# Performance work log

Hardware: AMD Instinct MI355X
Metric: run time of the kernel (lower is better)

The kernel has to match this reference:

```python
import jax, jax.numpy as jnp
import numpy as np
from jax import lax

B, H, W, CIN = 16, 96, 320, 32
N_ACTIVE = 200000
COUT = 256
FC_IN = (H // 8) * (W // 8) * 128  # 12*40*128 = 61440


def _conv(x, w, b):
    # stride-2, pad-1, 3x3 conv in NCHW / OIHW layout
    y = lax.conv_general_dilated(x, w, (2, 2), [(1, 1), (1, 1)],
                                 dimension_numbers=('NCHW', 'OIHW', 'NCHW'))
    return y + b[None, :, None, None]


def _maxpool3(x):
    # 3x3 maxpool, stride 1, pad 1 (NCHW)
    return lax.reduce_window(x, -jnp.inf, lax.max,
                             (1, 1, 3, 3), (1, 1, 1, 1),
                             [(0, 0), (0, 0), (1, 1), (1, 1)])


def setup_inputs() -> dict:
    key = jax.random.key(0)
    ks = jax.random.split(key, 12)
    input_feat = jax.random.normal(ks[0], (B, H, W, CIN), dtype=jnp.float32)
    cb = jax.random.randint(ks[1], (N_ACTIVE, 1), 0, B)
    cy = jax.random.randint(ks[2], (N_ACTIVE, 1), 0, H)
    cx = jax.random.randint(ks[3], (N_ACTIVE, 1), 0, W)
    spconv_coords = jnp.concatenate([cb, cy, cx], axis=1).astype(jnp.int32)
    w1 = jax.random.normal(ks[4], (32, CIN, 3, 3), dtype=jnp.float32) * (1.0 / np.sqrt(CIN * 9))
    b1 = jax.random.normal(ks[5], (32,), dtype=jnp.float32) * 0.01
    w2 = jax.random.normal(ks[6], (64, 32, 3, 3), dtype=jnp.float32) * (1.0 / np.sqrt(32 * 9))
    b2 = jax.random.normal(ks[7], (64,), dtype=jnp.float32) * 0.01
    w3 = jax.random.normal(ks[8], (128, 64, 3, 3), dtype=jnp.float32) * (1.0 / np.sqrt(64 * 9))
    b3 = jax.random.normal(ks[9], (128,), dtype=jnp.float32) * 0.01
    fc_w = jax.random.normal(ks[10], (COUT, FC_IN), dtype=jnp.float32) * (1.0 / np.sqrt(FC_IN))
    fc_b = jax.random.normal(ks[11], (COUT,), dtype=jnp.float32) * 0.01
    return {"input_feat": input_feat, "spconv_coords": spconv_coords,
            "w1": w1, "b1": b1, "w2": w2, "b2": b2, "w3": w3, "b3": b3,
            "fc_w": fc_w, "fc_b": fc_b}


def reference(input_feat, spconv_coords, w1, b1, w2, b2, w3, b3, fc_w, fc_b):
    bi = spconv_coords[:, 0]
    yi = spconv_coords[:, 1]
    xi = spconv_coords[:, 2]
    # gather active-site features, then scatter into a dense NHWC grid
    feats = input_feat[bi, yi, xi]                       # [N, CIN]
    dense = jnp.zeros_like(input_feat).at[bi, yi, xi].set(feats)
    x = dense.transpose(0, 3, 1, 2)                      # [B, CIN, H, W]
    x = jax.nn.relu(_maxpool3(_conv(x, w1, b1)))         # [B, 32, H/2, W/2]
    x = jax.nn.relu(_maxpool3(_conv(x, w2, b2)))         # [B, 64, H/4, W/4]
    x = jax.nn.relu(_maxpool3(_conv(x, w3, b3)))         # [B, 128, H/8, W/8]
    x = x.reshape(x.shape[0], -1)                        # [B, FC_IN]
    return jax.nn.relu(x @ fc_w.T + fc_b)                # [B, COUT]
```

## Files before the change

kernel.cpp:

```cpp
#include <hip/hip_runtime.h>

#define NB 16
#define NH 96
#define NW 320
#define NCIN 32

#define FC_K 61440
#define FC_KB 128
#define FC_NKC 480

typedef __attribute__((ext_vector_type(8))) short short8;
typedef __attribute__((ext_vector_type(4))) float f32x4;

__device__ inline unsigned short f2bf(float f) {
    union { float f; unsigned int u; } v; v.f = f;
    unsigned int r = v.u + 0x7FFF + ((v.u >> 16) & 1);
    return (unsigned short)(r >> 16);
}
__device__ inline float bf2f(unsigned short s) {
    union { unsigned int u; float f; } v; v.u = ((unsigned int)s) << 16; return v.f;
}
__device__ inline unsigned short fhi(float f) {
    union { float f; unsigned int u; } v; v.f = f; return (unsigned short)(v.u >> 16);
}

__global__ __launch_bounds__(256) void setup_all(const float* __restrict__ w1,
                                                 const float* __restrict__ w2,
                                                 const float* __restrict__ w3,
                                                 unsigned short* __restrict__ f1,
                                                 unsigned short* __restrict__ f2,
                                                 unsigned short* __restrict__ f3,
                                                 const int* __restrict__ coords,
                                                 const float* __restrict__ input,
                                                 unsigned short* __restrict__ inBf,
                                                 int n) {
    if (blockIdx.x < 396) {
        int i = blockIdx.x * 256 + threadIdx.x;
        if (i < 9216) {
            int j = i & 7, lane = (i >> 3) & 63, nt = (i >> 9) & 1, tap = i >> 10;
            int ic = ((lane >> 4) * 8) + j, oc = nt * 16 + (lane & 15);
            f1[i] = f2bf(w1[(oc * 32 + ic) * 9 + tap]);
        } else if (i < 27648) {
            int v = i - 9216;
            int j = v & 7, lane = (v >> 3) & 63, nt = (v >> 9) & 3, tap = v >> 11;
            int ic = ((lane >> 4) * 8) + j, oc = nt * 16 + (lane & 15);
            f2[v] = f2bf(w2[(oc * 32 + ic) * 9 + tap]);
        } else if (i < 101376) {
            int v = i - 27648;
            int j = v & 7, lane = (v >> 3) & 63, nt = (v >> 9) & 7, kk = v >> 12;
            int tap = kk >> 1, ks = kk & 1;
            int ic = ks * 32 + ((lane >> 4) * 8) + j, oc = nt * 16 + (lane & 15);
            f3[v] = f2bf(w3[(oc * 64 + ic) * 9 + tap]);
        }
    } else {
        int i = (blockIdx.x - 396) * 256 + threadIdx.x;
        if (i >= n * 4) return;
        int ci = i >> 2, q = i & 3;
        int b = coords[ci * 3 + 0], y = coords[ci * 3 + 1], x = coords[ci * 3 + 2];
        long base = ((long)((b * NH + y) * NW + x)) * NCIN + q * 8;
        const float4* src = (const float4*)(input + base);
        float4 v0 = src[0], v1 = src[1];
        union { short8 s8; unsigned short us[8]; } o;
        o.us[0] = f2bf(v0.x); o.us[1] = f2bf(v0.y); o.us[2] = f2bf(v0.z); o.us[3] = f2bf(v0.w);
        o.us[4] = f2bf(v1.x); o.us[5] = f2bf(v1.y); o.us[6] = f2bf(v1.z); o.us[7] = f2bf(v1.w);
        *(short8*)(inBf + base) = o.s8;
    }
}

template<int IC, int OC, int NTB, int TY, int TX, int IH, int IW, int OH, int OW>
__global__ __launch_bounds__(512) void convpool_mfma(
    const unsigned short* __restrict__ inPtr,
    const unsigned short* __restrict__ wfrag,
    const float* __restrict__ bias,
    unsigned short* __restrict__ outBf)
{
    constexpr int KS  = IC / 32;
    constexpr int NT  = OC / 16;
    constexpr int OCB = NTB * 16;
    constexpr int NOC = OC / OCB;
    constexpr int CY = TY + 2, CX = TX + 2;
    constexpr int NCELL  = CY * CX;
    constexpr int NSTRIP = (NCELL + 15) / 16;
    constexpr int CSS = OCB + 8;
    constexpr int NTY = OH / TY, NTX = OW / TX;

    __shared__ __align__(16) unsigned short cs[NCELL * CSS];

    int bid = blockIdx.x;
    const int ocsel = bid % NOC; bid /= NOC;
    const int txi = bid % NTX;   bid /= NTX;
    const int tyi = bid % NTY;
    const int b   = bid / NTY;
    const int y0 = tyi * TY, x0 = txi * TX;

    const int t = threadIdx.x;
    const int wid = t >> 6, lane = t & 63, quad = lane >> 4, lm = lane & 15;

    short8 zero8;
    #pragma unroll
    for (int j = 0; j < 8; j++) zero8[j] = 0;

    for (int s = wid; s < NSTRIP; s += 8) {
        int idx = s * 16 + lm;
        if (idx > NCELL - 1) idx = NCELL - 1;
        const int oy = y0 - 1 + idx / CX;
        const int ox = x0 - 1 + idx % CX;
        const int iy0 = oy * 2 - 1, ix0 = ox * 2 - 1;

        int cell[9]; bool okb[9];
        #pragma unroll
        for (int t9 = 0; t9 < 9; t9++) {
            const int iy = iy0 + t9 / 3;
            const int ix = ix0 + t9 % 3;
            const bool ok = (iy >= 0) && (iy < IH) && (ix >= 0) && (ix < IW);
            cell[t9] = ok ? ((b * IH + iy) * IW + ix) : 0;
            okb[t9] = ok;
        }

        f32x4 acc[NTB][2];
        #pragma unroll
        for (int nl = 0; nl < NTB; nl++)
            #pragma unroll
            for (int pp = 0; pp < 2; pp++)
                acc[nl][pp] = (f32x4){0.f, 0.f, 0.f, 0.f};

        #pragma unroll
        for (int ks = 0; ks < KS; ks++) {
            short8 av[9];
            #pragma unroll
            for (int t9 = 0; t9 < 9; t9++) {
                short8 v = *(const short8*)(inPtr + (long)cell[t9] * IC + ks * 32 + quad * 8);
                av[t9] = okb[t9] ? v : zero8;
            }
            #pragma unroll
            for (int nl = 0; nl < NTB; nl++) {
                const int nt = ocsel * NTB + nl;
                #pragma unroll
                for (int t9 = 0; t9 < 9; t9++) {
                    short8 bf = *(const short8*)(wfrag + (((t9 * KS + ks) * NT + nt) * 64 + lane) * 8);
                    if (t9 & 1) acc[nl][1] = __builtin_amdgcn_mfma_f32_16x16x32_bf16(av[t9], bf, acc[nl][1], 0, 0, 0);
                    else        acc[nl][0] = __builtin_amdgcn_mfma_f32_16x16x32_bf16(av[t9], bf, acc[nl][0], 0, 0, 0);
                }
            }
        }

        #pragma unroll
        for (int nl = 0; nl < NTB; nl++) {
            const float bv = bias[(ocsel * NTB + nl) * 16 + lm];
            #pragma unroll
            for (int reg = 0; reg < 4; reg++) {
                const int ci = s * 16 + quad * 4 + reg;
                if (ci < NCELL)
                    cs[ci * CSS + nl * 16 + lm] = f2bf(acc[nl][0][reg] + acc[nl][1][reg] + bv);
            }
        }
    }
    __syncthreads();

    constexpr int NTASK = TY * TX * (OCB / 8);
    for (int u = t; u < NTASK; u += 512) {
        const int c8 = u & (OCB / 8 - 1);
        const int px = (u / (OCB / 8)) % TX;
        const int py = u / ((OCB / 8) * TX);
        const int gy = y0 + py, gx = x0 + px;

        float m[8];
        #pragma unroll
        for (int e = 0; e < 8; e++) m[e] = 0.f;

        #pragma unroll
        for (int dy = -1; dy <= 1; dy++) {
            const int yy = gy + dy;
            if (yy < 0 || yy >= OH) continue;
            #pragma unroll
            for (int dx = -1; dx <= 1; dx++) {
                const int xx = gx + dx;
                if (xx < 0 || xx >= OW) continue;
                const int ci = (py + dy + 1) * CX + (px + dx + 1);
                short8 v = *(const short8*)(&cs[ci * CSS + c8 * 8]);
                #pragma unroll
                for (int e = 0; e < 8; e++)
                    m[e] = fmaxf(m[e], bf2f((unsigned short)v[e]));
            }
        }
        union { short8 s8; unsigned short us[8]; } o;
        #pragma unroll
        for (int e = 0; e < 8; e++) o.us[e] = fhi(m[e]);
        *(short8*)(outBf + ((long)((b * OH + gy) * OW + gx)) * OC + ocsel * OCB + c8 * 8) = o.s8;
    }
}

template<int IC, int OC, int NL, int IH, int IW, int OH, int OW>
__global__ __launch_bounds__(256) void conv_mfma(
    const unsigned short* __restrict__ inPtr,
    const unsigned short* __restrict__ wfrag,
    const float* __restrict__ bias,
    float* __restrict__ out)
{
    constexpr int KS = IC / 32;
    constexpr int NT = OC / 16;
    constexpr int NG = NT / NL;
    constexpr int NSTRIPS = NB * OH * OW / 16;

    const int wid  = (blockIdx.x * 256 + threadIdx.x) >> 6;
    const int lane = threadIdx.x & 63;
    const int ntb  = (wid % NG) * NL;
    const int s    = wid / NG;
    if (s >= NSTRIPS) return;
    const int quad = lane >> 4;
    const int lm   = lane & 15;

    const int p0 = s * 16;
    const int posA = p0 + lm;
    const int b  = posA / (OH * OW);
    const int rr = posA % (OH * OW);
    const int oy = rr / OW, ox = rr % OW;
    const int iy0 = oy * 2 - 1, ix0 = ox * 2 - 1;

    int cell[9];
    bool okb[9];
    #pragma unroll
    for (int t9 = 0; t9 < 9; t9++) {
        const int iy = iy0 + t9 / 3;
        const int ix = ix0 + t9 % 3;
        const bool ok = (iy >= 0) && (iy < IH) && (ix >= 0) && (ix < IW);
        cell[t9] = ok ? ((b * IH + iy) * IW + ix) : 0;
        okb[t9] = ok;
    }

    short8 zero8;
    #pragma unroll
    for (int j = 0; j < 8; j++) zero8[j] = 0;

    f32x4 acc[NL][2];
    #pragma unroll
    for (int nl = 0; nl < NL; nl++)
        #pragma unroll
        for (int pp = 0; pp < 2; pp++)
            acc[nl][pp] = (f32x4){0.f, 0.f, 0.f, 0.f};

    #pragma unroll 1
    for (int ks = 0; ks < KS; ks++) {
        short8 av[9];
        #pragma unroll
        for (int t9 = 0; t9 < 9; t9++) {
            short8 v = *(const short8*)(inPtr + (long)cell[t9] * IC + ks * 32 + quad * 8);
            av[t9] = okb[t9] ? v : zero8;
        }
        #pragma unroll
        for (int nl = 0; nl < NL; nl++) {
            #pragma unroll
            for (int t9 = 0; t9 < 9; t9++) {
                short8 bf = *(const short8*)(wfrag + (((t9 * KS + ks) * NT + ntb + nl) * 64 + lane) * 8);
                if (t9 & 1) acc[nl][1] = __builtin_amdgcn_mfma_f32_16x16x32_bf16(av[t9], bf, acc[nl][1], 0, 0, 0);
                else        acc[nl][0] = __builtin_amdgcn_mfma_f32_16x16x32_bf16(av[t9], bf, acc[nl][0], 0, 0, 0);
            }
        }
    }

    const long rowBase = (long)p0 + quad * 4;
    #pragma unroll
    for (int nl = 0; nl < NL; nl++) {
        const int oc = (ntb + nl) * 16 + lm;
        const float bv = bias[oc];
        #pragma unroll
        for (int reg = 0; reg < 4; reg++)
            out[(rowBase + reg) * OC + oc] = acc[nl][0][reg] + acc[nl][1][reg] + bv;
    }
}

__global__ __launch_bounds__(256) void pool_transpose(const float* __restrict__ conv3o,
                                                      float* __restrict__ xT) {
    __shared__ float tile_s[8 * 16 * 17];
    const int pt = blockIdx.x % 30;
    const int ct = blockIdx.x / 30;
    const int pos0 = pt * 16, c0 = ct * 8;
    const int t = threadIdx.x;
    {
        const int b = t >> 4, pl = t & 15;
        const int pos = pos0 + pl;
        const int py = pos / 40, px = pos % 40;
        float4 m0 = make_float4(0.f, 0.f, 0.f, 0.f);
        float4 m1 = make_float4(0.f, 0.f, 0.f, 0.f);
        #pragma unroll
        for (int dy = -1; dy <= 1; dy++) {
            const int yy = py + dy;
            if (yy < 0 || yy >= 12) continue;
            #pragma unroll
            for (int dx = -1; dx <= 1; dx++) {
                const int xx = px + dx;
                if (xx < 0 || xx >= 40) continue;
                const float4* src = (const float4*)(conv3o + ((long)((b * 12 + yy) * 40 + xx)) * 128 + c0);
                float4 v0 = src[0], v1 = src[1];
                m0.x = fmaxf(m0.x, v0.x); m0.y = fmaxf(m0.y, v0.y);
                m0.z = fmaxf(m0.z, v0.z); m0.w = fmaxf(m0.w, v0.w);
                m1.x = fmaxf(m1.x, v1.x); m1.y = fmaxf(m1.y, v1.y);
                m1.z = fmaxf(m1.z, v1.z); m1.w = fmaxf(m1.w, v1.w);
            }
        }
        tile_s[(0 * 16 + pl) * 17 + b] = m0.x;
        tile_s[(1 * 16 + pl) * 17 + b] = m0.y;
        tile_s[(2 * 16 + pl) * 17 + b] = m0.z;
        tile_s[(3 * 16 + pl) * 17 + b] = m0.w;
        tile_s[(4 * 16 + pl) * 17 + b] = m1.x;
        tile_s[(5 * 16 + pl) * 17 + b] = m1.y;
        tile_s[(6 * 16 + pl) * 17 + b] = m1.z;
        tile_s[(7 * 16 + pl) * 17 + b] = m1.w;
    }
    __syncthreads();
    {
        const int w = t >> 6, l = t & 63;
        const int pl2 = l >> 2, b4 = l & 3;
        #pragma unroll
        for (int i = 0; i < 2; i++) {
            int cl = w + 4 * i;
            const float* ls = &tile_s[(cl * 16 + pl2) * 17 + 4 * b4];
            float4 v = make_float4(ls[0], ls[1], ls[2], ls[3]);
            *(float4*)(xT + ((long)(c0 + cl) * 480 + pos0 + pl2) * 16 + 4 * b4) = v;
        }
    }
}

__global__ __launch_bounds__(512, 4) void fc_main(const float* __restrict__ xT,
                                                  const float* __restrict__ fw,
                                                  float* __restrict__ partial)
{
    __shared__ float x_lds[128 * 20];
    const int kc   = blockIdx.x;
    const int t    = threadIdx.x;
    const int q    = t >> 2;
    const int ksub = t & 3;
    const int k0   = kc * FC_KB;

    {
        const int kr = t >> 2, b4 = t & 3;
        *(float4*)(&x_lds[kr * 20 + b4 * 4]) =
            *(const float4*)(xT + ((long)(k0 + kr)) * 16 + b4 * 4);
    }
    __syncthreads();

    float acc[2][16];
    #pragma unroll
    for (int s = 0; s < 2; s++)
        #pragma unroll
        for (int b = 0; b < 16; b++) acc[s][b] = 0.f;

    const float* wbase = fw + (long)q * FC_K + k0 + ksub * 4;

    #pragma unroll
    for (int p = 0; p < 2; p++) {
        f32x4 w[2][4];
        #pragma unroll
        for (int s = 0; s < 2; s++) {
            const float* wr = wbase + (long)s * (128 * FC_K) + p * 64;
            #pragma unroll
            for (int j = 0; j < 4; j++)
                w[s][j] = *(const f32x4*)(wr + j * 16);
        }
        #pragma unroll
        for (int j = 0; j < 4; j++) {
            #pragma unroll
            for (int e = 0; e < 4; e++) {
                const int row = p * 64 + j * 16 + ksub * 4 + e;
                const float* xr = &x_lds[row * 20];
                f32x4 xv[4];
                #pragma unroll
                for (int b4 = 0; b4 < 4; b4++)
                    xv[b4] = *(const f32x4*)(xr + 4 * b4);
                #pragma unroll
                for (int s = 0; s < 2; s++) {
                    const float wv = w[s][j][e];
                    #pragma unroll
                    for (int b4 = 0; b4 < 4; b4++)
                        #pragma unroll
                        for (int el = 0; el < 4; el++)
                            acc[s][b4 * 4 + el] = fmaf(wv, xv[b4][el], acc[s][b4 * 4 + el]);
                }
            }
        }
    }

    #pragma unroll
    for (int s = 0; s < 2; s++)
        #pragma unroll
        for (int b = 0; b < 16; b++) {
            float v = acc[s][b];
            v += __shfl_xor(v, 1);
            v += __shfl_xor(v, 2);
            acc[s][b] = v;
        }

    if (ksub == 0) {
        #pragma unroll
        for (int s = 0; s < 2; s++) {
            const int oc = q + 128 * s;
            float4* pp = (float4*)(partial + ((long)kc * 256 + oc) * 16);
            pp[0] = make_float4(acc[s][0],  acc[s][1],  acc[s][2],  acc[s][3]);
            pp[1] = make_float4(acc[s][4],  acc[s][5],  acc[s][6],  acc[s][7]);
            pp[2] = make_float4(acc[s][8],  acc[s][9],  acc[s][10], acc[s][11]);
            pp[3] = make_float4(acc[s][12], acc[s][13], acc[s][14], acc[s][15]);
        }
    }
}

__global__ __launch_bounds__(256) void fc_reduce(const float* __restrict__ partial,
                                                 const float* __restrict__ fcb,
                                                 float* __restrict__ out)
{
    __shared__ float red[16][17];
    const int oc = blockIdx.x;
    const int ol = threadIdx.x & 15;
    const int st = threadIdx.x >> 4;
    float s = 0.f;
    #pragma unroll 5
    for (int j = 0; j < 30; j++)
        s += partial[(long)(st + 16 * j) * 4096 + oc * 16 + ol];
    red[st][ol] = s;
    __syncthreads();
    if (threadIdx.x < 16) {
        float tot = fcb[oc];
        #pragma unroll
        for (int k = 0; k < 16; k++) tot += red[k][threadIdx.x];
        out[threadIdx.x * 256 + oc] = fmaxf(tot, 0.f);
    }
}

extern "C" void kernel_launch(void* const* d_in, const int* in_sizes, int n_in,
                              void* d_out, int out_size, void* d_ws, size_t ws_size,
                              hipStream_t stream) {
    const float* input  = (const float*)d_in[0];
    const int*   coords = (const int*)d_in[1];
    const float* w1 = (const float*)d_in[2];
    const float* b1 = (const float*)d_in[3];
    const float* w2 = (const float*)d_in[4];
    const float* b2 = (const float*)d_in[5];
    const float* w3 = (const float*)d_in[6];
    const float* b3 = (const float*)d_in[7];
    const float* fcw = (const float*)d_in[8];
    const float* fcb = (const float*)d_in[9];
    float* outp = (float*)d_out;

    const int n_active = in_sizes[1] / 3;

    char* ws = (char*)d_ws;
    unsigned short* wf1 = (unsigned short*)ws;
    unsigned short* wf2 = wf1 + 9216;
    unsigned short* wf3 = wf2 + 18432;
    unsigned short* inBf    = (unsigned short*)(ws + 204800);
    unsigned short* pool1bf = (unsigned short*)(ws + 31662080);
    unsigned short* pool2bf = (unsigned short*)(ws + 39526400);
    float*          conv3o  = (float*)(ws + 43458560);
    float*          xT      = (float*)(ws + 47390720);
    float*          partial = (float*)(ws + 51322880);

    hipMemsetAsync(inBf, 0, 31457280, stream);
    const int scatterBlocks = (n_active * 4 + 255) / 256;
    setup_all<<<396 + scatterBlocks, 256, 0, stream>>>(w1, w2, w3, wf1, wf2, wf3,
                                                       coords, input, inBf, n_active);

    convpool_mfma<32, 32, 2, 16, 16, 96, 320, 48, 160>
        <<<480, 512, 0, stream>>>(inBf, wf1, b1, pool1bf);

    convpool_mfma<32, 64, 2, 8, 16, 48, 160, 24, 80>
        <<<480, 512, 0, stream>>>(pool1bf, wf2, b2, pool2bf);

    conv_mfma<64, 128, 1, 24, 80, 12, 40>
        <<<960, 256, 0, stream>>>(pool2bf, wf3, b3, conv3o);

    pool_transpose<<<480, 256, 0, stream>>>(conv3o, xT);

    fc_main<<<FC_NKC, 512, 0, stream>>>(xT, fcw, partial);
    fc_reduce<<<256, 256, 0, stream>>>(partial, fcb, outp);
}
```

Baseline: 231.4 us.

## Double-buffer FC weights into LDS via async global_load_lds with XOR swizzle

The FC kernel now streams its weight tile into a double-buffered LDS region using direct global-to-LDS loads, staging the next 32-column chunk while computing on the current one. A XOR swizzle on the 16-byte groups is meant to avoid LDS bank conflicts when threads read their weight rows back. This replaces per-thread strided global loads, aiming to coalesce traffic and overlap memory with FMA work. In exchange it adds 64KB of LDS per block, which limits occupancy, plus extra barriers every stage.

```diff
diff --git a/kernel.cpp b/kernel.cpp
--- a/kernel.cpp
+++ b/kernel.cpp
@@ -22,6 +22,12 @@
 }
 __device__ inline unsigned short fhi(float f) {
     union { float f; unsigned int u; } v; v.f = f; return (unsigned short)(v.u >> 16);
+}
+
+__device__ inline void gload_lds16(const float* gsrc, float* lds_dst) {
+    __builtin_amdgcn_global_load_lds(
+        (const __attribute__((address_space(1))) unsigned int*)gsrc,
+        (__attribute__((address_space(3))) unsigned int*)lds_dst, 16, 0, 0);
 }
 
 __global__ __launch_bounds__(256) void setup_all(const float* __restrict__ w1,
@@ -325,6 +331,7 @@
                                                   const float* __restrict__ fw,
                                                   float* __restrict__ partial)
 {
+    __shared__ float wbuf[2][8192];
     __shared__ float x_lds[128 * 20];
     const int kc   = blockIdx.x;
     const int t    = threadIdx.x;
@@ -332,11 +339,23 @@
     const int ksub = t & 3;
     const int k0   = kc * FC_KB;
 
+    #define FC_STAGE(pp)                                                       \
+        _Pragma("unroll")                                                      \
+        for (int i = 0; i < 4; i++) {                                          \
+            const int c = i * 512 + t;                                         \
+            const int r = c >> 3;                                              \
+            const int g = (c & 7) ^ (r & 7);                                   \
+            gload_lds16(fw + (long)r * FC_K + k0 + (pp) * 32 + g * 4,          \
+                        &wbuf[(pp) & 1][c * 4]);                               \
+        }
+
+    FC_STAGE(0);
     {
         const int kr = t >> 2, b4 = t & 3;
         *(float4*)(&x_lds[kr * 20 + b4 * 4]) =
             *(const float4*)(xT + ((long)(k0 + kr)) * 16 + b4 * 4);
     }
+    asm volatile("s_waitcnt vmcnt(0)" ::: "memory");
     __syncthreads();
 
     float acc[2][16];
@@ -345,40 +364,39 @@
         #pragma unroll
         for (int b = 0; b < 16; b++) acc[s][b] = 0.f;
 
-    const float* wbase = fw + (long)q * FC_K + k0 + ksub * 4;
-
-    #pragma unroll
-    for (int p = 0; p < 2; p++) {
-        f32x4 w[2][4];
-        #pragma unroll
-        for (int s = 0; s < 2; s++) {
-            const float* wr = wbase + (long)s * (128 * FC_K) + p * 64;
-            #pragma unroll
-            for (int j = 0; j < 4; j++)
-                w[s][j] = *(const f32x4*)(wr + j * 16);
-        }
-        #pragma unroll
-        for (int j = 0; j < 4; j++) {
+    const int h = q & 7;
+
+    #pragma unroll
+    for (int p = 0; p < 4; p++) {
+        if (p < 3) { FC_STAGE(p + 1); }
+
+        const float* wb = wbuf[p & 1];
+        #pragma unroll
+        for (int j = 0; j < 2; j++) {
+            const int gp = (ksub + 4 * j) ^ h;
+            const f32x4 w0 = *(const f32x4*)(wb + q * 32 + gp * 4);
+            const f32x4 w1 = *(const f32x4*)(wb + (q + 128) * 32 + gp * 4);
             #pragma unroll
             for (int e = 0; e < 4; e++) {
-                const int row = p * 64 + j * 16 + ksub * 4 + e;
+                const int row = p * 32 + j * 16 + ksub * 4 + e;
                 const float* xr = &x_lds[row * 20];
                 f32x4 xv[4];
                 #pragma unroll
                 for (int b4 = 0; b4 < 4; b4++)
                     xv[b4] = *(const f32x4*)(xr + 4 * b4);
                 #pragma unroll
-                for (int s = 0; s < 2; s++) {
-                    const float wv = w[s][j][e];
+                for (int b4 = 0; b4 < 4; b4++)
                     #pragma unroll
-                    for (int b4 = 0; b4 < 4; b4++)
-                        #pragma unroll
-                        for (int el = 0; el < 4; el++)
-                            acc[s][b4 * 4 + el] = fmaf(wv, xv[b4][el], acc[s][b4 * 4 + el]);
-                }
-            }
-        }
-    }
+                    for (int el = 0; el < 4; el++) {
+                        acc[0][b4 * 4 + el] = fmaf(w0[e], xv[b4][el], acc[0][b4 * 4 + el]);
+                        acc[1][b4 * 4 + el] = fmaf(w1[e], xv[b4][el], acc[1][b4 * 4 + el]);
+                    }
+            }
+        }
+        asm volatile("s_waitcnt vmcnt(0)" ::: "memory");
+        __syncthreads();
+    }
+    #undef FC_STAGE
 
     #pragma unroll
     for (int s = 0; s < 2; s++)
```

New measurement: 255.2 us. 10.3% more time.
